# Performance work log

Measured on AMD Instinct MI355X. Metric: run time of the kernel, lower is better.

## Reference

```python
import jax, jax.numpy as jnp
import numpy as np

# ProbLog program semantics, closed-form:
# Grid 2x2, cell index = 2*X + Y: 0=(0,0), 1=(0,1), 2=(1,0), 3=(1,1).
# Actions (query order): 0=stay, 1=up, 2=down, 3=left, 4=right.
# transition/5 only defines clauses for stay/up/down (plus west/east which never
# unify with left/right), so left/right can never produce 'unsafe'.
# unsafe :- pacman(X,Y), action(A), transition(X,Y,A,X1,Y1), ghost(X1,Y1).
# evidence(safe) conditions the action query: P(a|safe) = p_a(a)*safe(a)/sum.

def _build_T():
    T = np.zeros((5, 4, 4), dtype=np.float32)  # [action, pac_cell, ghost_cell]
    for c in range(4):
        T[0, c, c] = 1.0  # stay
    # up: (x,y)->(x,y+1): cell0->1, cell2->3 (y=1 cells move off-grid -> no ghost)
    T[1, 0, 1] = 1.0
    T[1, 2, 3] = 1.0
    # down: (x,y)->(x,y-1): cell1->0, cell3->2
    T[2, 1, 0] = 1.0
    T[2, 3, 2] = 1.0
    # left/right: no transition clauses -> always safe
    return T

_T = _build_T()


def setup_inputs() -> dict:
    key = jax.random.key(0)
    ks = jax.random.split(key, 4)
    B, H = 16384, 2048
    s = 1.0 / np.sqrt(H)
    return {
        "x": jax.random.normal(ks[0], (B, H), dtype=jnp.float32),
        "Wg": jax.random.normal(ks[1], (H, 4), dtype=jnp.float32) * s,
        "bg": jnp.zeros((4,), dtype=jnp.float32),
        "Wp": jax.random.normal(ks[2], (H, 4), dtype=jnp.float32) * s,
        "bp": jnp.zeros((4,), dtype=jnp.float32),
        "Wa": jax.random.normal(ks[3], (H, 5), dtype=jnp.float32) * s,
        "ba": jnp.zeros((5,), dtype=jnp.float32),
    }


def reference(x, Wg, bg, Wp, bp, Wa, ba):
    ghost = jax.nn.softmax(x @ Wg + bg, axis=-1)   # [B,4]
    pacman = jax.nn.softmax(x @ Wp + bp, axis=-1)  # [B,4]
    base = jax.nn.softmax(x @ Wa + ba, axis=-1)    # [B,5]
    T = jnp.asarray(_T)                            # [5,4,4]
    # P(unsafe | action=a) = sum_c pac[c] * ghost[target(c,a)]
    unsafe = jnp.einsum('bc,acd,bd->ba', pacman, T, ghost)  # [B,5]
    joint = base * (1.0 - unsafe)                  # P(action=a, safe)
    return joint / jnp.sum(joint, axis=-1, keepdims=True)   # P(action=a | safe)
```

## Files before the change

kernel.cpp:

```cpp
#include <hip/hip_runtime.h>
#include <hip/hip_fp16.h>


typedef __fp16 h2_t __attribute__((ext_vector_type(2)));
typedef __fp16 h4_t __attribute__((ext_vector_type(4)));

__global__ __launch_bounds__(256, 2)
void dpl_safe_policy_kernel(const float* __restrict__ x,
                            const float* __restrict__ Wg, const float* __restrict__ bg,
                            const float* __restrict__ Wp, const float* __restrict__ bp,
                            const float* __restrict__ Wa, const float* __restrict__ ba,
                            float* __restrict__ out)
{
    __shared__ __align__(16) __fp16 wlds[13 * 2048];

    const int tid = threadIdx.x;

    const float4* Wg4 = (const float4*)Wg;
    const float4* Wp4 = (const float4*)Wp;
    for (int h = tid; h < 2048; h += 256) {
        float4 g = Wg4[h];
        wlds[0 * 2048 + h] = (__fp16)g.x;
        wlds[1 * 2048 + h] = (__fp16)g.y;
        wlds[2 * 2048 + h] = (__fp16)g.z;
        wlds[3 * 2048 + h] = (__fp16)g.w;
        float4 p = Wp4[h];
        wlds[4 * 2048 + h] = (__fp16)p.x;
        wlds[5 * 2048 + h] = (__fp16)p.y;
        wlds[6 * 2048 + h] = (__fp16)p.z;
        wlds[7 * 2048 + h] = (__fp16)p.w;
        #pragma unroll
        for (int j = 0; j < 5; ++j)
            wlds[(8 + j) * 2048 + h] = (__fp16)Wa[h * 5 + j];
    }
    __syncthreads();

    const int w  = tid >> 6;
    const int l  = tid & 63;
    const int hs = l & 15;
    const int rg = l >> 4;
    const int rowbase = blockIdx.x * 32 + w * 8;
    const int row0 = rowbase + rg * 2;

    const float4* xg = (const float4*)x;
    const long b0 = (long)row0 * 512 + hs;
    const long b1 = b0 + 512;

    const h4_t* w4 = (const h4_t*)wlds;

    float acc0[13], acc1[13];
    #pragma unroll
    for (int j = 0; j < 13; ++j) { acc0[j] = 0.f; acc1[j] = 0.f; }

    float4 c00 = xg[b0],      c10 = xg[b1];
    float4 c01 = xg[b0 + 16], c11 = xg[b1 + 16];

    #pragma unroll 2
    for (int c = 0; c < 32; ++c) {
        const float4 xv0 = c00, xv1 = c10;
        c00 = c01; c10 = c11;
        if (c + 2 < 32) {
            c01 = xg[b0 + (c + 2) * 16];
            c11 = xg[b1 + (c + 2) * 16];
        }
        const h2_t xl0 = __builtin_amdgcn_cvt_pkrtz(xv0.x, xv0.y);
        const h2_t xh0 = __builtin_amdgcn_cvt_pkrtz(xv0.z, xv0.w);
        const h2_t xl1 = __builtin_amdgcn_cvt_pkrtz(xv1.x, xv1.y);
        const h2_t xh1 = __builtin_amdgcn_cvt_pkrtz(xv1.z, xv1.w);
        const int wb = c * 16 + hs;
        #pragma unroll
        for (int j = 0; j < 13; ++j) {
            const h4_t wv = w4[j * 512 + wb];
            const h2_t wlo = __builtin_shufflevector(wv, wv, 0, 1);
            const h2_t whi = __builtin_shufflevector(wv, wv, 2, 3);
#if __has_builtin(__builtin_amdgcn_fdot2)
            acc0[j] = __builtin_amdgcn_fdot2(xl0, wlo, acc0[j], false);
            acc0[j] = __builtin_amdgcn_fdot2(xh0, whi, acc0[j], false);
            acc1[j] = __builtin_amdgcn_fdot2(xl1, wlo, acc1[j], false);
            acc1[j] = __builtin_amdgcn_fdot2(xh1, whi, acc1[j], false);
#else
            acc0[j] += (float)xl0.x * (float)wlo.x + (float)xl0.y * (float)wlo.y
                     + (float)xh0.x * (float)whi.x + (float)xh0.y * (float)whi.y;
            acc1[j] += (float)xl1.x * (float)wlo.x + (float)xl1.y * (float)wlo.y
                     + (float)xh1.x * (float)whi.x + (float)xh1.y * (float)whi.y;
#endif
        }
    }

    #pragma unroll
    for (int j = 0; j < 13; ++j) {
        acc0[j] += __shfl_xor(acc0[j], 1, 64);
        acc0[j] += __shfl_xor(acc0[j], 2, 64);
        acc0[j] += __shfl_xor(acc0[j], 4, 64);
        acc0[j] += __shfl_xor(acc0[j], 8, 64);
        acc1[j] += __shfl_xor(acc1[j], 1, 64);
        acc1[j] += __shfl_xor(acc1[j], 2, 64);
        acc1[j] += __shfl_xor(acc1[j], 4, 64);
        acc1[j] += __shfl_xor(acc1[j], 8, 64);
    }

    const float vbg0 = bg[0], vbg1 = bg[1], vbg2 = bg[2], vbg3 = bg[3];
    const float vbp0 = bp[0], vbp1 = bp[1], vbp2 = bp[2], vbp3 = bp[3];
    const float vba0 = ba[0], vba1 = ba[1], vba2 = ba[2], vba3 = ba[3], vba4 = ba[4];

    #pragma unroll
    for (int r = 0; r < 2; ++r) {
        const float* acc = r ? acc1 : acc0;
        const float g0 = acc[0] + vbg0, g1 = acc[1] + vbg1, g2 = acc[2] + vbg2, g3 = acc[3] + vbg3;
        const float q0 = acc[4] + vbp0, q1 = acc[5] + vbp1, q2 = acc[6] + vbp2, q3 = acc[7] + vbp3;
        const float a0 = acc[8] + vba0, a1 = acc[9] + vba1, a2 = acc[10] + vba2,
                    a3 = acc[11] + vba3, a4 = acc[12] + vba4;

        float m, s, inv;
        m = fmaxf(fmaxf(g0, g1), fmaxf(g2, g3));
        const float eg0 = __expf(g0 - m), eg1 = __expf(g1 - m), eg2 = __expf(g2 - m), eg3 = __expf(g3 - m);
        s = eg0 + eg1 + eg2 + eg3; inv = 1.f / s;
        const float G0 = eg0 * inv, G1 = eg1 * inv, G2 = eg2 * inv, G3 = eg3 * inv;

        m = fmaxf(fmaxf(q0, q1), fmaxf(q2, q3));
        const float ep0 = __expf(q0 - m), ep1 = __expf(q1 - m), ep2 = __expf(q2 - m), ep3 = __expf(q3 - m);
        s = ep0 + ep1 + ep2 + ep3; inv = 1.f / s;
        const float P0 = ep0 * inv, P1 = ep1 * inv, P2 = ep2 * inv, P3 = ep3 * inv;

        m = fmaxf(fmaxf(fmaxf(a0, a1), fmaxf(a2, a3)), a4);
        const float ea0 = __expf(a0 - m), ea1 = __expf(a1 - m), ea2 = __expf(a2 - m),
                    ea3 = __expf(a3 - m), ea4 = __expf(a4 - m);
        s = ea0 + ea1 + ea2 + ea3 + ea4; inv = 1.f / s;
        const float A0 = ea0 * inv, A1 = ea1 * inv, A2 = ea2 * inv, A3 = ea3 * inv, A4 = ea4 * inv;

        const float u0 = P0 * G0 + P1 * G1 + P2 * G2 + P3 * G3;
        const float u1 = P0 * G1 + P2 * G3;
        const float u2 = P1 * G0 + P3 * G2;

        const float j0 = A0 * (1.f - u0), j1 = A1 * (1.f - u1), j2 = A2 * (1.f - u2),
                    j3 = A3, j4 = A4;
        const float isd = 1.f / (j0 + j1 + j2 + j3 + j4);

        if (hs < 5) {
            const float ov = (hs == 0) ? j0 : (hs == 1) ? j1 : (hs == 2) ? j2 : (hs == 3) ? j3 : j4;
            out[(row0 + r) * 5 + hs] = ov * isd;
        }
    }
}

extern "C" void kernel_launch(void* const* d_in, const int* in_sizes, int n_in,
                              void* d_out, int out_size, void* d_ws, size_t ws_size,
                              hipStream_t stream) {
    const float* x  = (const float*)d_in[0];
    const float* Wg = (const float*)d_in[1];
    const float* bg = (const float*)d_in[2];
    const float* Wp = (const float*)d_in[3];
    const float* bp = (const float*)d_in[4];
    const float* Wa = (const float*)d_in[5];
    const float* ba = (const float*)d_in[6];
    float* out = (float*)d_out;

    const int B = in_sizes[0] / 2048;
    const int grid = B / 32;
    dpl_safe_policy_kernel<<<grid, 256, 0, stream>>>(x, Wg, bg, Wp, bp, Wa, ba, out);
}
```

Measured before the change: 210.2 us.

## Split K across blocks with prepacked fp16 weights and a separate reduce epilogue

Splits the single fused kernel into three: a one-time weight pack to fp16 in workspace, a split-K partial GEMM over 4 H-slices (2048 blocks, smaller LDS, all x loads issued up front), and a reduce kernel that sums partials and applies the softmax/safety epilogue. The aim is to cut the per-block LDS weight conversion cost and raise occupancy and memory-level parallelism for streaming the 128 MB x. In exchange it adds two extra launches and a round-trip of partial sums through global memory. It also relies on a hardcoded B=16384 in the partial indexing.

```diff
diff --git a/kernel.cpp b/kernel.cpp
--- a/kernel.cpp
+++ b/kernel.cpp
@@ -1,37 +1,45 @@
 #include <hip/hip_runtime.h>
-#include <hip/hip_fp16.h>
 
 
 typedef __fp16 h2_t __attribute__((ext_vector_type(2)));
 typedef __fp16 h4_t __attribute__((ext_vector_type(4)));
 
-__global__ __launch_bounds__(256, 2)
-void dpl_safe_policy_kernel(const float* __restrict__ x,
-                            const float* __restrict__ Wg, const float* __restrict__ bg,
-                            const float* __restrict__ Wp, const float* __restrict__ bp,
-                            const float* __restrict__ Wa, const float* __restrict__ ba,
-                            float* __restrict__ out)
+#define WS_PART_OFF 65536
+
+__global__ void pack_weights(const float* __restrict__ Wg,
+                             const float* __restrict__ Wp,
+                             const float* __restrict__ Wa,
+                             __fp16* __restrict__ wout)
 {
-    __shared__ __align__(16) __fp16 wlds[13 * 2048];
+    const int t = blockIdx.x * 256 + threadIdx.x;
+    const int j = t >> 11, h = t & 2047;
+    const int s = h >> 9, hk = h & 511;
+    float v;
+    if (j < 4)      v = Wg[h * 4 + j];
+    else if (j < 8) v = Wp[h * 4 + (j - 4)];
+    else            v = Wa[h * 5 + (j - 8)];
+    wout[s * 6656 + j * 512 + hk] = (__fp16)v;
+}
+
+__global__ __launch_bounds__(256, 4)
+void gemm_partial(const float* __restrict__ x,
+                  const __fp16* __restrict__ wpk,
+                  float* __restrict__ part)
+{
+    __shared__ __align__(16) __fp16 wl[13 * 512];
 
     const int tid = threadIdx.x;
+    const int rt  = blockIdx.x & 511;
+    const int s   = blockIdx.x >> 9;
 
-    const float4* Wg4 = (const float4*)Wg;
-    const float4* Wp4 = (const float4*)Wp;
-    for (int h = tid; h < 2048; h += 256) {
-        float4 g = Wg4[h];
-        wlds[0 * 2048 + h] = (__fp16)g.x;
-        wlds[1 * 2048 + h] = (__fp16)g.y;
-        wlds[2 * 2048 + h] = (__fp16)g.z;
-        wlds[3 * 2048 + h] = (__fp16)g.w;
-        float4 p = Wp4[h];
-        wlds[4 * 2048 + h] = (__fp16)p.x;
-        wlds[5 * 2048 + h] = (__fp16)p.y;
-        wlds[6 * 2048 + h] = (__fp16)p.z;
-        wlds[7 * 2048 + h] = (__fp16)p.w;
-        #pragma unroll
-        for (int j = 0; j < 5; ++j)
-            wlds[(8 + j) * 2048 + h] = (__fp16)Wa[h * 5 + j];
+    {
+        const uint4* src = (const uint4*)(wpk + s * 6656);
+        uint4* dst = (uint4*)wl;
+        int i = tid;
+        dst[i] = src[i]; i += 256;
+        dst[i] = src[i]; i += 256;
+        dst[i] = src[i]; i += 256;
+        if (i < 832) dst[i] = src[i];
     }
     __syncthreads();
 
@@ -39,38 +47,35 @@
     const int l  = tid & 63;
     const int hs = l & 15;
     const int rg = l >> 4;
-    const int rowbase = blockIdx.x * 32 + w * 8;
-    const int row0 = rowbase + rg * 2;
+    const int row0 = rt * 32 + w * 8 + rg * 2;
 
     const float4* xg = (const float4*)x;
-    const long b0 = (long)row0 * 512 + hs;
+    const long b0 = (long)row0 * 512 + s * 128 + hs;
     const long b1 = b0 + 512;
 
-    const h4_t* w4 = (const h4_t*)wlds;
+    float4 xa[8], xb[8];
+    #pragma unroll
+    for (int c = 0; c < 8; ++c) {
+        xa[c] = xg[b0 + c * 16];
+        xb[c] = xg[b1 + c * 16];
+    }
 
     float acc0[13], acc1[13];
     #pragma unroll
     for (int j = 0; j < 13; ++j) { acc0[j] = 0.f; acc1[j] = 0.f; }
 
-    float4 c00 = xg[b0],      c10 = xg[b1];
-    float4 c01 = xg[b0 + 16], c11 = xg[b1 + 16];
+    const h4_t* w4 = (const h4_t*)wl;
 
-    #pragma unroll 2
-    for (int c = 0; c < 32; ++c) {
-        const float4 xv0 = c00, xv1 = c10;
-        c00 = c01; c10 = c11;
-        if (c + 2 < 32) {
-            c01 = xg[b0 + (c + 2) * 16];
-            c11 = xg[b1 + (c + 2) * 16];
-        }
-        const h2_t xl0 = __builtin_amdgcn_cvt_pkrtz(xv0.x, xv0.y);
-        const h2_t xh0 = __builtin_amdgcn_cvt_pkrtz(xv0.z, xv0.w);
-        const h2_t xl1 = __builtin_amdgcn_cvt_pkrtz(xv1.x, xv1.y);
-        const h2_t xh1 = __builtin_amdgcn_cvt_pkrtz(xv1.z, xv1.w);
+    #pragma unroll
+    for (int c = 0; c < 8; ++c) {
+        const h2_t xl0 = __builtin_amdgcn_cvt_pkrtz(xa[c].x, xa[c].y);
+        const h2_t xh0 = __builtin_amdgcn_cvt_pkrtz(xa[c].z, xa[c].w);
+        const h2_t xl1 = __builtin_amdgcn_cvt_pkrtz(xb[c].x, xb[c].y);
+        const h2_t xh1 = __builtin_amdgcn_cvt_pkrtz(xb[c].z, xb[c].w);
         const int wb = c * 16 + hs;
         #pragma unroll
         for (int j = 0; j < 13; ++j) {
-            const h4_t wv = w4[j * 512 + wb];
+            const h4_t wv = w4[j * 128 + wb];
             const h2_t wlo = __builtin_shufflevector(wv, wv, 0, 1);
             const h2_t whi = __builtin_shufflevector(wv, wv, 2, 3);
 #if __has_builtin(__builtin_amdgcn_fdot2)
@@ -99,48 +104,68 @@
         acc1[j] += __shfl_xor(acc1[j], 8, 64);
     }
 
-    const float vbg0 = bg[0], vbg1 = bg[1], vbg2 = bg[2], vbg3 = bg[3];
-    const float vbp0 = bp[0], vbp1 = bp[1], vbp2 = bp[2], vbp3 = bp[3];
-    const float vba0 = ba[0], vba1 = ba[1], vba2 = ba[2], vba3 = ba[3], vba4 = ba[4];
+    float v0 = acc0[12], v1 = acc1[12];
+    #pragma unroll
+    for (int j = 11; j >= 0; --j) {
+        v0 = (hs == j) ? acc0[j] : v0;
+        v1 = (hs == j) ? acc1[j] : v1;
+    }
+    if (hs < 13) {
+        const long pbase = ((long)(s << 14) + row0) * 13;
+        part[pbase + hs]      = v0;
+        part[pbase + 13 + hs] = v1;
+    }
+}
 
+__global__ __launch_bounds__(256)
+void reduce_epilogue(const float* __restrict__ part,
+                     const float* __restrict__ bg, const float* __restrict__ bp,
+                     const float* __restrict__ ba, float* __restrict__ out)
+{
+    const int r = blockIdx.x * 256 + threadIdx.x;
+
+    float acc[13];
     #pragma unroll
-    for (int r = 0; r < 2; ++r) {
-        const float* acc = r ? acc1 : acc0;
-        const float g0 = acc[0] + vbg0, g1 = acc[1] + vbg1, g2 = acc[2] + vbg2, g3 = acc[3] + vbg3;
-        const float q0 = acc[4] + vbp0, q1 = acc[5] + vbp1, q2 = acc[6] + vbp2, q3 = acc[7] + vbp3;
-        const float a0 = acc[8] + vba0, a1 = acc[9] + vba1, a2 = acc[10] + vba2,
-                    a3 = acc[11] + vba3, a4 = acc[12] + vba4;
+    for (int j = 0; j < 13; ++j) acc[j] = 0.f;
+    #pragma unroll
+    for (int s = 0; s < 4; ++s) {
+        const long pbase = ((long)(s << 14) + r) * 13;
+        #pragma unroll
+        for (int j = 0; j < 13; ++j) acc[j] += part[pbase + j];
+    }
 
-        float m, s, inv;
-        m = fmaxf(fmaxf(g0, g1), fmaxf(g2, g3));
-        const float eg0 = __expf(g0 - m), eg1 = __expf(g1 - m), eg2 = __expf(g2 - m), eg3 = __expf(g3 - m);
-        s = eg0 + eg1 + eg2 + eg3; inv = 1.f / s;
-        const float G0 = eg0 * inv, G1 = eg1 * inv, G2 = eg2 * inv, G3 = eg3 * inv;
+    const float g0 = acc[0] + bg[0], g1 = acc[1] + bg[1], g2 = acc[2] + bg[2], g3 = acc[3] + bg[3];
+    const float q0 = acc[4] + bp[0], q1 = acc[5] + bp[1], q2 = acc[6] + bp[2], q3 = acc[7] + bp[3];
+    const float a0 = acc[8] + ba[0], a1 = acc[9] + ba[1], a2 = acc[10] + ba[2],
+                a3 = acc[11] + ba[3], a4 = acc[12] + ba[4];
 
-        m = fmaxf(fmaxf(q0, q1), fmaxf(q2, q3));
-        const float ep0 = __expf(q0 - m), ep1 = __expf(q1 - m), ep2 = __expf(q2 - m), ep3 = __expf(q3 - m);
-        s = ep0 + ep1 + ep2 + ep3; inv = 1.f / s;
-        const float P0 = ep0 * inv, P1 = ep1 * inv, P2 = ep2 * inv, P3 = ep3 * inv;
+    float m, sum, inv;
+    m = fmaxf(fmaxf(g0, g1), fmaxf(g2, g3));
+    const float eg0 = __expf(g0 - m), eg1 = __expf(g1 - m), eg2 = __expf(g2 - m), eg3 = __expf(g3 - m);
+    sum = eg0 + eg1 + eg2 + eg3; inv = 1.f / sum;
+    const float G0 = eg0 * inv, G1 = eg1 * inv, G2 = eg2 * inv, G3 = eg3 * inv;
 
-        m = fmaxf(fmaxf(fmaxf(a0, a1), fmaxf(a2, a3)), a4);
-        const float ea0 = __expf(a0 - m), ea1 = __expf(a1 - m), ea2 = __expf(a2 - m),
-                    ea3 = __expf(a3 - m), ea4 = __expf(a4 - m);
-        s = ea0 + ea1 + ea2 + ea3 + ea4; inv = 1.f / s;
-        const float A0 = ea0 * inv, A1 = ea1 * inv, A2 = ea2 * inv, A3 = ea3 * inv, A4 = ea4 * inv;
+    m = fmaxf(fmaxf(q0, q1), fmaxf(q2, q3));
+    const float ep0 = __expf(q0 - m), ep1 = __expf(q1 - m), ep2 = __expf(q2 - m), ep3 = __expf(q3 - m);
+    sum = ep0 + ep1 + ep2 + ep3; inv = 1.f / sum;
+    const float P0 = ep0 * inv, P1 = ep1 * inv, P2 = ep2 * inv, P3 = ep3 * inv;
 
-        const float u0 = P0 * G0 + P1 * G1 + P2 * G2 + P3 * G3;
-        const float u1 = P0 * G1 + P2 * G3;
-        const float u2 = P1 * G0 + P3 * G2;
+    m = fmaxf(fmaxf(fmaxf(a0, a1), fmaxf(a2, a3)), a4);
+    const float ea0 = __expf(a0 - m), ea1 = __expf(a1 - m), ea2 = __expf(a2 - m),
+                ea3 = __expf(a3 - m), ea4 = __expf(a4 - m);
+    sum = ea0 + ea1 + ea2 + ea3 + ea4; inv = 1.f / sum;
+    const float A0 = ea0 * inv, A1 = ea1 * inv, A2 = ea2 * inv, A3 = ea3 * inv, A4 = ea4 * inv;
 
-        const float j0 = A0 * (1.f - u0), j1 = A1 * (1.f - u1), j2 = A2 * (1.f - u2),
-                    j3 = A3, j4 = A4;
-        const float isd = 1.f / (j0 + j1 + j2 + j3 + j4);
+    const float u0 = P0 * G0 + P1 * G1 + P2 * G2 + P3 * G3;
+    const float u1 = P0 * G1 + P2 * G3;
+    const float u2 = P1 * G0 + P3 * G2;
 
-        if (hs < 5) {
-            const float ov = (hs == 0) ? j0 : (hs == 1) ? j1 : (hs == 2) ? j2 : (hs == 3) ? j3 : j4;
-            out[(row0 + r) * 5 + hs] = ov * isd;
-        }
-    }
+    const float j0 = A0 * (1.f - u0), j1 = A1 * (1.f - u1), j2 = A2 * (1.f - u2),
+                j3 = A3, j4 = A4;
+    const float isd = 1.f / (j0 + j1 + j2 + j3 + j4);
+
+    float* o = out + (long)r * 5;
+    o[0] = j0 * isd; o[1] = j1 * isd; o[2] = j2 * isd; o[3] = j3 * isd; o[4] = j4 * isd;
 }
 
 extern "C" void kernel_launch(void* const* d_in, const int* in_sizes, int n_in,
@@ -155,7 +180,10 @@
     const float* ba = (const float*)d_in[6];
     float* out = (float*)d_out;
 
-    const int B = in_sizes[0] / 2048;
-    const int grid = B / 32;
-    dpl_safe_policy_kernel<<<grid, 256, 0, stream>>>(x, Wg, bg, Wp, bp, Wa, ba, out);
+    __fp16* wpk = (__fp16*)d_ws;
+    float* part = (float*)((char*)d_ws + WS_PART_OFF);
+
+    pack_weights<<<104, 256, 0, stream>>>(Wg, Wp, Wa, wpk);
+    gemm_partial<<<2048, 256, 0, stream>>>(x, wpk, part);
+    reduce_epilogue<<<64, 256, 0, stream>>>(part, bg, bp, ba, out);
 }
```

New measurement: 206.8 us. No clear change (-1.6%).
